# Kernel tuning notes

Measured on AMD Instinct MI355X. Metric: run time of the kernel, lower is better.

## Reference

```python
import jax, jax.numpy as jnp
import numpy as np

G = 4          # n_groups
KG = 1         # kernel_groups[stage]
KS = 8         # kernel_sizes[stage]
EIN = 64       # eff_in_dim = in_dim // n_groups
EOUT = 64      # eff_out_dim
PIN = 32       # in_points
POUT = 128     # out_points
QD = 256       # query_dim
EPS = 1e-5


def _ln(x, axes):
    m = jnp.mean(x, axis=axes, keepdims=True)
    v = jnp.var(x, axis=axes, keepdims=True)
    return (x - m) * jax.lax.rsqrt(v + EPS)


def setup_inputs() -> dict:
    key = jax.random.key(0)
    ks = jax.random.split(key, 14)
    B, N = 8, 300
    s = 0.02
    common_out = G * (EIN * EOUT + PIN * POUT)  # 32768
    priv_out = 2 * G * KG * KS * KS             # 512
    flat = EOUT * POUT * G                      # 32768
    return {
        "stage": 0,
        "x": jax.random.normal(ks[0], (B, N, G, PIN, EIN), jnp.float32),
        "query": jax.random.normal(ks[1], (B, N, QD), jnp.float32),
        "cpg_w": jax.random.normal(ks[2], (common_out, QD), jnp.float32) * s,
        "cpg_b": jax.random.normal(ks[3], (common_out,), jnp.float32) * s,
        "ppg_w": jax.random.normal(ks[4], (priv_out, QD), jnp.float32) * s,
        "ppg_b": jax.random.normal(ks[5], (priv_out,), jnp.float32) * s,
        "ml": jax.random.normal(ks[6], (G * KG, EIN, KS), jnp.float32) * 0.1,
        "mr": jax.random.normal(ks[7], (G * KG, KS, EOUT), jnp.float32) * 0.1,
        "sl": jax.random.normal(ks[8], (G * KG, POUT, KS), jnp.float32) * 0.1,
        "sr": jax.random.normal(ks[9], (G * KG, KS, PIN), jnp.float32) * 0.1,
        "base_w": jax.random.normal(ks[10], (QD, flat), jnp.float32) * s,
        "lora_A": jax.random.normal(ks[11], (64, flat), jnp.float32) * s,
        "lora_B": jax.random.normal(ks[12], (QD, 64), jnp.float32) * s,
        "out_bias": jnp.zeros((QD,), jnp.float32),
        "gamma": jnp.ones((QD,), jnp.float32),
        "beta": jnp.zeros((QD,), jnp.float32),
    }


def reference(stage, x, query, cpg_w, cpg_b, ppg_w, ppg_b, ml, mr, sl, sr,
              base_w, lora_A, lora_B, out_bias, gamma, beta):
    B, N, g, P, C = x.shape
    BN = B * N
    q = query.reshape(BN, QD)

    # common (query-generated) mixing params
    common = (q @ cpg_w.T + cpg_b).reshape(BN, G, EIN * EOUT + PIN * POUT)
    Mc = common[..., : EIN * EOUT].reshape(BN, G, EIN, EOUT)
    Sc = common[..., EIN * EOUT :].reshape(BN, G, POUT, PIN)

    # private factorized params: ml @ mz @ mr, sl @ sz @ sr
    priv = (q @ ppg_w.T + ppg_b).reshape(BN, 2, G * KG, KS, KS)
    mz, sz = priv[:, 0], priv[:, 1]
    Mp = jnp.einsum("gik,bgkl,glj->bgij", ml, mz, mr)  # (BN, G*KG, EIN, EOUT)
    Sp = jnp.einsum("gik,bgkl,glj->bgij", sl, sz, sr)  # (BN, G*KG, POUT, PIN)

    M = Mc + Mp.reshape(BN, G, KG, EIN, EOUT).sum(axis=2)
    S = Sc + Sp.reshape(BN, G, KG, POUT, PIN).sum(axis=2)

    out = x.reshape(BN, G, P, C)
    # adaptive channel mixing + LN over last two dims + ReLU
    out = jnp.einsum("bgpc,bgcd->bgpd", out, M)
    out = jax.nn.relu(_ln(out, (-2, -1)))
    # adaptive spatial mixing + LN + ReLU
    out = jnp.einsum("bgop,bgpd->bgod", S, out)  # (BN, G, POUT, EOUT)
    out = jax.nn.relu(_ln(out, (-2, -1)))

    # low-rank-adjusted linear projection to query dim
    out = out.reshape(B, N, G * POUT * EOUT)
    W = base_w + lora_B @ lora_A  # (QD, flat)
    out = out @ W.T + out_bias

    # residual + affine LayerNorm
    y = query + out
    return _ln(y, (-1,)) * gamma + beta
```

## Files before the change

kernel.cpp:

```cpp
#include <hip/hip_runtime.h>
#include <hip/hip_bf16.h>

#define BN_TOK 2400
#define QDIM   256
#define NG     4
#define FLAT   32768
#define GSZ    8192
#define KSP    16
#define LN_EPS 1e-5f
#define PPAD   42

typedef __attribute__((ext_vector_type(8))) short bf16x8;
typedef __attribute__((ext_vector_type(4))) float f32x4;
typedef __hip_bfloat16 bf16;

__device__ __forceinline__ float bf2f(ushort u) {
  union { unsigned int i; float f; } c;
  c.i = ((unsigned int)u) << 16;
  return c.f;
}
__device__ __forceinline__ ushort f2u(float f) {
  bf16 h = __float2bfloat16(f);
  union { bf16 h; ushort u; } c; c.h = h; return c.u;
}

__device__ __forceinline__ int xcdswz(int orig, int nwg) {
  int xcd = orig & 7, base = orig >> 3;
  int q = nwg >> 3, r = nwg & 7;
  int start = (xcd < r) ? xcd * (q + 1) : r * (q + 1) + (xcd - r) * q;
  return start + base;
}

__global__ __launch_bounds__(256) void cast_k(const float* __restrict__ in,
                                              bf16* __restrict__ out, int n4) {
  int i = blockIdx.x * 256 + threadIdx.x;
  if (i < n4) {
    float4 v = ((const float4*)in)[i];
    bf16 tmp[4] = {__float2bfloat16(v.x), __float2bfloat16(v.y),
                   __float2bfloat16(v.z), __float2bfloat16(v.w)};
    ((ushort4*)out)[i] = *(const ushort4*)tmp;
  }
}

__global__ __launch_bounds__(256) void build_weff_k(
    const float* __restrict__ cpg_w, const float* __restrict__ cpg_b,
    const float* __restrict__ ppg_w, const float* __restrict__ ppg_b,
    const float* __restrict__ ml, const float* __restrict__ mr,
    const float* __restrict__ sl, const float* __restrict__ sr,
    bf16* __restrict__ Weff, float* __restrict__ bias_eff) {
  int tid = threadIdx.x;
  int rb = blockIdx.x;
  int g = blockIdx.y;
  int part = blockIdx.z;
  int pbase = part * 256 + g * 64;

  float pw[64];
#pragma unroll
  for (int kl = 0; kl < 64; ++kl)
    pw[kl] = ppg_w[(size_t)(pbase + kl) * QDIM + tid];

  if (part == 0) {
    int d = rb;
    float t[8];
#pragma unroll
    for (int k = 0; k < 8; ++k) {
      float s = 0.f;
#pragma unroll
      for (int l = 0; l < 8; ++l) s += mr[g * 512 + l * 64 + d] * pw[k * 8 + l];
      t[k] = s;
    }
    for (int r = 0; r < 64; ++r) {
      int outrow = g * GSZ + d * 64 + r;
      int srcrow = g * GSZ + r * 64 + d;
      float acc = cpg_w[(size_t)srcrow * QDIM + tid];
#pragma unroll
      for (int k = 0; k < 8; ++k) acc += ml[g * 512 + r * 8 + k] * t[k];
      Weff[(size_t)outrow * QDIM + tid] = __float2bfloat16(acc);
    }
    if (tid < 64) {
      int r = tid;
      float b = cpg_b[g * GSZ + r * 64 + d];
#pragma unroll
      for (int k = 0; k < 8; ++k) {
        float s = 0.f;
#pragma unroll
        for (int l = 0; l < 8; ++l)
          s += mr[g * 512 + l * 64 + d] * ppg_b[pbase + k * 8 + l];
        b += ml[g * 512 + r * 8 + k] * s;
      }
      bias_eff[g * GSZ + d * 64 + r] = b;
    }
  } else {
    int o0 = rb * 2;
    float t0v[8], t1v[8];
#pragma unroll
    for (int l = 0; l < 8; ++l) {
      float s0 = 0.f, s1 = 0.f;
#pragma unroll
      for (int k = 0; k < 8; ++k) {
        s0 += sl[g * 1024 + o0 * 8 + k] * pw[k * 8 + l];
        s1 += sl[g * 1024 + (o0 + 1) * 8 + k] * pw[k * 8 + l];
      }
      t0v[l] = s0; t1v[l] = s1;
    }
    for (int r = 0; r < 32; ++r) {
      int rr = rb * 64 + r;
      int p = rr & 31;
      int row = g * GSZ + 4096 + rr;
      float acc = cpg_w[(size_t)row * QDIM + tid];
#pragma unroll
      for (int l = 0; l < 8; ++l) acc += sr[g * 256 + l * 32 + p] * t0v[l];
      Weff[(size_t)row * QDIM + tid] = __float2bfloat16(acc);
    }
    for (int r = 32; r < 64; ++r) {
      int rr = rb * 64 + r;
      int p = rr & 31;
      int row = g * GSZ + 4096 + rr;
      float acc = cpg_w[(size_t)row * QDIM + tid];
#pragma unroll
      for (int l = 0; l < 8; ++l) acc += sr[g * 256 + l * 32 + p] * t1v[l];
      Weff[(size_t)row * QDIM + tid] = __float2bfloat16(acc);
    }
    if (tid < 64) {
      int rr = rb * 64 + tid;
      int o = rr >> 5, p = rr & 31;
      int row = g * GSZ + 4096 + rr;
      float b = cpg_b[row];
#pragma unroll
      for (int l = 0; l < 8; ++l) {
        float s = 0.f;
#pragma unroll
        for (int k = 0; k < 8; ++k)
          s += sl[g * 1024 + o * 8 + k] * ppg_b[pbase + k * 8 + l];
        b += sr[g * 256 + l * 32 + p] * s;
      }
      bias_eff[row] = b;
    }
  }
}

__global__ __launch_bounds__(256) void build_wb_k(
    const float* __restrict__ base_w, const float* __restrict__ lora_A,
    const float* __restrict__ lora_B, bf16* __restrict__ Wb) {
  int jb = blockIdx.x * 256;
  int i0 = blockIdx.y * 16;
  int tid = threadIdx.x;
  __shared__ float lB[16][64];
  for (int e = tid; e < 16 * 64; e += 256)
    lB[e >> 6][e & 63] = lora_B[(size_t)(i0 + (e >> 6)) * 64 + (e & 63)];
  __syncthreads();
  int j = jb + tid;
  float acc[16] = {};
  for (int r = 0; r < 64; ++r) {
    float la = lora_A[(size_t)r * FLAT + j];
#pragma unroll
    for (int i = 0; i < 16; ++i) acc[i] += lB[i][r] * la;
  }
#pragma unroll
  for (int i = 0; i < 16; ++i)
    Wb[(size_t)(i0 + i) * FLAT + j] =
        __float2bfloat16(base_w[(size_t)(i0 + i) * FLAT + j] + acc[i]);
}

template <bool OBF>
__global__ __launch_bounds__(256) void gemm_nt(
    const bf16* __restrict__ A, const bf16* __restrict__ B,
    const float* __restrict__ bias, void* __restrict__ Cout,
    int M, int lda, int ldb, int Kslice, int ldc) {
  __shared__ __align__(16) ushort smem[16384];
  ushort* As = smem;
  ushort* Bs = smem + 8192;
  int tid = threadIdx.x;
  int w = tid >> 6, lane = tid & 63;
  int nwg = gridDim.x * gridDim.y;
  int swz = xcdswz(blockIdx.x + gridDim.x * blockIdx.y, nwg);
  int m0 = (swz % gridDim.x) * 128, n0 = (swz / gridDim.x) * 128;
  int kbase = blockIdx.z * Kslice;
  int wm = (w & 1) * 64, wn = (w >> 1) * 64;
  f32x4 acc[4][4] = {};
  for (int kb = 0; kb < Kslice; kb += 64) {
#pragma unroll
    for (int i = 0; i < 4; ++i) {
      int c = (i * 4 + w) * 64 + lane;
      int row = c >> 3, slot = c & 7;
      int ss = slot ^ (row & 7);
      int grow = m0 + row; if (grow >= M) grow = M - 1;
      const bf16* srcA = A + (size_t)grow * lda + kbase + kb + ss * 8;
      __builtin_amdgcn_global_load_lds(
          (const __attribute__((address_space(1))) void*)srcA,
          (__attribute__((address_space(3))) void*)(As + (size_t)c * 8), 16, 0, 0);
      const bf16* srcB = B + (size_t)(n0 + row) * ldb + kbase + kb + ss * 8;
      __builtin_amdgcn_global_load_lds(
          (const __attribute__((address_space(1))) void*)srcB,
          (__attribute__((address_space(3))) void*)(Bs + (size_t)c * 8), 16, 0, 0);
    }
    __syncthreads();
#pragma unroll
    for (int ks = 0; ks < 2; ++ks) {
      int sl = ks * 4 + (lane >> 4);
      bf16x8 af[4], bfr[4];
#pragma unroll
      for (int i = 0; i < 4; ++i) {
        int r = wm + i * 16 + (lane & 15);
        af[i] = *(const bf16x8*)&As[r * 64 + (sl ^ (r & 7)) * 8];
        int cc = wn + i * 16 + (lane & 15);
        bfr[i] = *(const bf16x8*)&Bs[cc * 64 + (sl ^ (cc & 7)) * 8];
      }
#pragma unroll
      for (int i = 0; i < 4; ++i)
#pragma unroll
        for (int j = 0; j < 4; ++j)
          acc[i][j] = __builtin_amdgcn_mfma_f32_16x16x32_bf16(bfr[j], af[i], acc[i][j], 0, 0, 0);
    }
    __syncthreads();
  }

  if constexpr (OBF) {
#pragma unroll
    for (int i = 0; i < 4; ++i) {
      int row = wm + i * 16 + (lane & 15);
#pragma unroll
      for (int j = 0; j < 4; ++j) {
        int nl = wn + j * 16 + (lane >> 4) * 4;
        float4 b4 = bias ? *(const float4*)&bias[n0 + nl] : make_float4(0.f, 0.f, 0.f, 0.f);
        ushort4 uv = {f2u(acc[i][j][0] + b4.x), f2u(acc[i][j][1] + b4.y),
                      f2u(acc[i][j][2] + b4.z), f2u(acc[i][j][3] + b4.w)};
        *(ushort4*)&smem[row * 128 + (nl ^ ((row & 7) << 3))] = uv;
      }
    }
    __syncthreads();
    bf16* co = (bf16*)Cout;
#pragma unroll
    for (int it = 0; it < 8; ++it) {
      int row = it * 16 + (tid >> 4);
      int sub = (tid & 15) * 8;
      int gm = m0 + row;
      if (gm < M) {
        *(bf16x8*)(co + ((size_t)blockIdx.z * M + gm) * ldc + n0 + sub) =
            *(const bf16x8*)&smem[row * 128 + (sub ^ ((row & 7) << 3))];
      }
    }
  } else {
#pragma unroll
    for (int i = 0; i < 4; ++i) {
      int m = m0 + wm + i * 16 + (lane & 15);
      if (m >= M) continue;
      size_t ro = (size_t)blockIdx.z * M + m;
#pragma unroll
      for (int j = 0; j < 4; ++j) {
        int nb = n0 + wn + j * 16 + (lane >> 4) * 4;
        float4 b4 = bias ? *(const float4*)&bias[nb] : make_float4(0.f, 0.f, 0.f, 0.f);
        *(float4*)((float*)Cout + ro * ldc + nb) =
            make_float4(acc[i][j][0] + b4.x, acc[i][j][1] + b4.y,
                        acc[i][j][2] + b4.z, acc[i][j][3] + b4.w);
      }
    }
  }
}

__device__ __forceinline__ void block_red2(float& s, float& sq, float* redS,
                                           float* redQ, int tid) {
#pragma unroll
  for (int off = 32; off > 0; off >>= 1) {
    s += __shfl_down(s, off);
    sq += __shfl_down(sq, off);
  }
  int w = tid >> 6;
  if ((tid & 63) == 0) { redS[w] = s; redQ[w] = sq; }
  __syncthreads();
  s = redS[0] + redS[1] + redS[2] + redS[3];
  sq = redQ[0] + redQ[1] + redQ[2] + redQ[3];
}

__global__ __launch_bounds__(256) void chain_k(
    const float* __restrict__ x, bf16* __restrict__ common) {
  int tid = threadIdx.x;
  int tl = blockIdx.x;
  int g = blockIdx.y;
  int lane = tid & 63, w = tid >> 6;

  __shared__ __align__(16) ushort sm[14720];
  __shared__ float redS[4], redQ[4];
  ushort* Mt = sm;
  ushort* Ss = sm + 4608;
  ushort* xbs = sm + 9728;
  ushort* o1Tb = sm + 12032;

  bf16* cm = common + (size_t)tl * FLAT + g * GSZ;
  const ushort* cmu = (const ushort*)cm;
  const float* xg = x + ((size_t)tl * NG + g) * 2048;

#pragma unroll
  for (int it = 0; it < 2; ++it) {
    int idx = it * 256 + tid;
    int e = idx * 8;
    {
      bf16x8 v = *(const bf16x8*)&cmu[e];
      *(bf16x8*)&Mt[(e >> 6) * 72 + (e & 63)] = v;
    }
    {
      bf16x8 v = *(const bf16x8*)&cmu[4096 + e];
      *(bf16x8*)&Ss[(e >> 5) * 40 + (e & 31)] = v;
    }
    {
      int fi = it * 256 + tid;
      float4 v = ((const float4*)xg)[fi];
      int fl = fi * 4;
      ushort4 u = {f2u(v.x), f2u(v.y), f2u(v.z), f2u(v.w)};
      *(ushort4*)&xbs[(fl >> 6) * 72 + (fl & 63)] = u;
    }
  }
  __syncthreads();

  int dlane = w * 16 + (lane & 15);
  f32x4 a1[2] = {};
#pragma unroll
  for (int ks = 0; ks < 2; ++ks) {
    bf16x8 af = *(const bf16x8*)&Mt[dlane * 72 + ks * 32 + (lane >> 4) * 8];
#pragma unroll
    for (int pt = 0; pt < 2; ++pt) {
      int p = pt * 16 + (lane & 15);
      bf16x8 bx = *(const bf16x8*)&xbs[p * 72 + ks * 32 + (lane >> 4) * 8];
      a1[pt] = __builtin_amdgcn_mfma_f32_16x16x32_bf16(af, bx, a1[pt], 0, 0, 0);
    }
  }
  {
    float s = 0.f, sq = 0.f;
#pragma unroll
    for (int pt = 0; pt < 2; ++pt)
#pragma unroll
      for (int r = 0; r < 4; ++r) { float v = a1[pt][r]; s += v; sq += v * v; }
    block_red2(s, sq, redS, redQ, tid);
    float mean = s * (1.f / 2048.f);
    float var = sq * (1.f / 2048.f) - mean * mean;
    float rs = rsqrtf(var + LN_EPS);
#pragma unroll
    for (int pt = 0; pt < 2; ++pt)
#pragma unroll
      for (int r = 0; r < 4; ++r) {
        float v = (a1[pt][r] - mean) * rs;
        if (v < 0.f) v = 0.f;
        int d = w * 16 + (lane >> 4) * 4 + r;
        int p = pt * 16 + (lane & 15);
        o1Tb[d * PPAD + p] = f2u(v);
      }
  }
  __syncthreads();

  f32x4 a2[2][4] = {};
  {
    bf16x8 bfd[4];
#pragma unroll
    for (int dj = 0; dj < 4; ++dj)
      bfd[dj] = *(const bf16x8*)&o1Tb[(dj * 16 + (lane & 15)) * PPAD + (lane >> 4) * 8];
#pragma unroll
    for (int oi = 0; oi < 2; ++oi) {
      int o = (2 * w + oi) * 16 + (lane & 15);
      bf16x8 sf = *(const bf16x8*)&Ss[o * 40 + (lane >> 4) * 8];
#pragma unroll
      for (int dj = 0; dj < 4; ++dj)
        a2[oi][dj] = __builtin_amdgcn_mfma_f32_16x16x32_bf16(bfd[dj], sf, a2[oi][dj], 0, 0, 0);
    }
  }
  {
    float s = 0.f, sq = 0.f;
#pragma unroll
    for (int oi = 0; oi < 2; ++oi)
#pragma unroll
      for (int dj = 0; dj < 4; ++dj)
#pragma unroll
        for (int r = 0; r < 4; ++r) { float v = a2[oi][dj][r]; s += v; sq += v * v; }
    block_red2(s, sq, redS, redQ, tid);
    float mean = s * (1.f / 8192.f);
    float var = sq * (1.f / 8192.f) - mean * mean;
    float rs = rsqrtf(var + LN_EPS);
#pragma unroll
    for (int oi = 0; oi < 2; ++oi) {
      int o = (2 * w + oi) * 16 + (lane & 15);
#pragma unroll
      for (int dj = 0; dj < 4; ++dj) {
        int d0 = dj * 16 + (lane >> 4) * 4;
        ushort4 uv;
#pragma unroll
        for (int r = 0; r < 4; ++r) {
          float v = (a2[oi][dj][r] - mean) * rs;
          if (v < 0.f) v = 0.f;
          ((ushort*)&uv)[r] = f2u(v);
        }
        *(ushort4*)&sm[o * 72 + d0] = uv;
      }
    }
  }
  __syncthreads();
  {
    ushort* cw = (ushort*)cm;
#pragma unroll
    for (int it = 0; it < 4; ++it) {
      int e = (it * 256 + tid) * 8;
      *(bf16x8*)&cw[e] = *(const bf16x8*)&sm[(e >> 6) * 72 + (e & 63)];
    }
  }
}

__global__ __launch_bounds__(256) void finish_k(
    const float* __restrict__ partial, const float* __restrict__ query,
    const float* __restrict__ out_bias, const float* __restrict__ gamma,
    const float* __restrict__ beta, float* __restrict__ out, int t0, int M) {
  int tid = threadIdx.x;
  int tl = blockIdx.x;
  int t = t0 + tl;
  __shared__ float redS[4], redQ[4];
  float s = 0.f;
  for (int ks = 0; ks < KSP; ++ks)
    s += partial[((size_t)ks * M + tl) * QDIM + tid];
  float v = s + out_bias[tid] + query[(size_t)t * QDIM + tid];
  float sum = v, sqv = v * v;
  block_red2(sum, sqv, redS, redQ, tid);
  float mean = sum * (1.f / 256.f);
  float var = sqv * (1.f / 256.f) - mean * mean;
  out[(size_t)t * QDIM + tid] =
      (v - mean) * rsqrtf(var + LN_EPS) * gamma[tid] + beta[tid];
}

extern "C" void kernel_launch(void* const* d_in, const int* in_sizes, int n_in,
                              void* d_out, int out_size, void* d_ws, size_t ws_size,
                              hipStream_t stream) {
  const float* x       = (const float*)d_in[1];
  const float* query   = (const float*)d_in[2];
  const float* cpg_w   = (const float*)d_in[3];
  const float* cpg_b   = (const float*)d_in[4];
  const float* ppg_w   = (const float*)d_in[5];
  const float* ppg_b   = (const float*)d_in[6];
  const float* ml      = (const float*)d_in[7];
  const float* mr      = (const float*)d_in[8];
  const float* sl      = (const float*)d_in[9];
  const float* sr      = (const float*)d_in[10];
  const float* base_w  = (const float*)d_in[11];
  const float* lora_A  = (const float*)d_in[12];
  const float* lora_B  = (const float*)d_in[13];
  const float* out_bias= (const float*)d_in[14];
  const float* gamma   = (const float*)d_in[15];
  const float* beta    = (const float*)d_in[16];
  float* out = (float*)d_out;

  float* wsf = (float*)d_ws;
  bf16*  Wb      = (bf16*)(wsf + 0);
  bf16*  Weff    = (bf16*)(wsf + 4194304);
  float* bias_eff= wsf + 8388608;
  bf16*  qb      = (bf16*)(wsf + 8421376);
  size_t fixedF  = 8728576;
  int CT = (ws_size >= (fixedF + (size_t)BN_TOK * 20480) * sizeof(float)) ? BN_TOK : 600;
  int NCH = BN_TOK / CT;
  bf16*  commonb = (bf16*)(wsf + fixedF);
  float* partialb= wsf + fixedF + (size_t)CT * 16384;

  build_weff_k<<<dim3(64, NG, 2), 256, 0, stream>>>(
      cpg_w, cpg_b, ppg_w, ppg_b, ml, mr, sl, sr, Weff, bias_eff);
  cast_k<<<dim3(BN_TOK * QDIM / 4 / 256), 256, 0, stream>>>(query, qb, BN_TOK * QDIM / 4);
  build_wb_k<<<dim3(FLAT / 256, QDIM / 16), 256, 0, stream>>>(base_w, lora_A, lora_B, Wb);

  for (int ch = 0; ch < NCH; ++ch) {
    int t0 = ch * CT;
    gemm_nt<true><<<dim3((CT + 127) / 128, FLAT / 128, 1), 256, 0, stream>>>(
        qb + (size_t)t0 * QDIM, Weff, bias_eff, commonb, CT, QDIM, QDIM, QDIM, FLAT);
    chain_k<<<dim3(CT, NG), 256, 0, stream>>>(x + (size_t)t0 * GSZ, commonb);
    gemm_nt<false><<<dim3((CT + 127) / 128, QDIM / 128, KSP), 256, 0, stream>>>(
        commonb, Wb, nullptr, partialb, CT, FLAT, FLAT, FLAT / KSP, QDIM);
    finish_k<<<dim3(CT), 256, 0, stream>>>(partialb, query, out_bias, gamma, beta, out, t0, CT);
  }
}
```

Before: 284.6 us.

## Enlarge GEMM tile to 256x128 and double split-K factor

```diff
diff --git a/kernel.cpp b/kernel.cpp
--- a/kernel.cpp
+++ b/kernel.cpp
@@ -6,7 +6,7 @@
 #define NG     4
 #define FLAT   32768
 #define GSZ    8192
-#define KSP    16
+#define KSP    32
 #define LN_EPS 1e-5f
 #define PPAD   42
 
@@ -167,20 +167,20 @@
     const bf16* __restrict__ A, const bf16* __restrict__ B,
     const float* __restrict__ bias, void* __restrict__ Cout,
     int M, int lda, int ldb, int Kslice, int ldc) {
-  __shared__ __align__(16) ushort smem[16384];
+  __shared__ __align__(16) ushort smem[24576];
   ushort* As = smem;
-  ushort* Bs = smem + 8192;
+  ushort* Bs = smem + 16384;
   int tid = threadIdx.x;
   int w = tid >> 6, lane = tid & 63;
   int nwg = gridDim.x * gridDim.y;
   int swz = xcdswz(blockIdx.x + gridDim.x * blockIdx.y, nwg);
-  int m0 = (swz % gridDim.x) * 128, n0 = (swz / gridDim.x) * 128;
+  int m0 = (swz % gridDim.x) * 256, n0 = (swz / gridDim.x) * 128;
   int kbase = blockIdx.z * Kslice;
-  int wm = (w & 1) * 64, wn = (w >> 1) * 64;
-  f32x4 acc[4][4] = {};
+  f32x4 acc[4][8] = {};
+
   for (int kb = 0; kb < Kslice; kb += 64) {
 #pragma unroll
-    for (int i = 0; i < 4; ++i) {
+    for (int i = 0; i < 8; ++i) {
       int c = (i * 4 + w) * 64 + lane;
       int row = c >> 3, slot = c & 7;
       int ss = slot ^ (row & 7);
@@ -189,6 +189,12 @@
       __builtin_amdgcn_global_load_lds(
           (const __attribute__((address_space(1))) void*)srcA,
           (__attribute__((address_space(3))) void*)(As + (size_t)c * 8), 16, 0, 0);
+    }
+#pragma unroll
+    for (int i = 0; i < 4; ++i) {
+      int c = (i * 4 + w) * 64 + lane;
+      int row = c >> 3, slot = c & 7;
+      int ss = slot ^ (row & 7);
       const bf16* srcB = B + (size_t)(n0 + row) * ldb + kbase + kb + ss * 8;
       __builtin_amdgcn_global_load_lds(
           (const __attribute__((address_space(1))) void*)srcB,
@@ -198,18 +204,21 @@
 #pragma unroll
     for (int ks = 0; ks < 2; ++ks) {
       int sl = ks * 4 + (lane >> 4);
-      bf16x8 af[4], bfr[4];
+      bf16x8 af[4], bfr[8];
 #pragma unroll
       for (int i = 0; i < 4; ++i) {
-        int r = wm + i * 16 + (lane & 15);
+        int r = w * 64 + i * 16 + (lane & 15);
         af[i] = *(const bf16x8*)&As[r * 64 + (sl ^ (r & 7)) * 8];
-        int cc = wn + i * 16 + (lane & 15);
-        bfr[i] = *(const bf16x8*)&Bs[cc * 64 + (sl ^ (cc & 7)) * 8];
+      }
+#pragma unroll
+      for (int j = 0; j < 8; ++j) {
+        int cc = j * 16 + (lane & 15);
+        bfr[j] = *(const bf16x8*)&Bs[cc * 64 + (sl ^ (cc & 7)) * 8];
       }
 #pragma unroll
       for (int i = 0; i < 4; ++i)
 #pragma unroll
-        for (int j = 0; j < 4; ++j)
+        for (int j = 0; j < 8; ++j)
           acc[i][j] = __builtin_amdgcn_mfma_f32_16x16x32_bf16(bfr[j], af[i], acc[i][j], 0, 0, 0);
     }
     __syncthreads();
@@ -217,38 +226,45 @@
 
   if constexpr (OBF) {
 #pragma unroll
+    for (int h = 0; h < 2; ++h) {
+      if ((w >> 1) == h) {
+        int wl = w & 1;
+#pragma unroll
+        for (int i = 0; i < 4; ++i) {
+          int row = wl * 64 + i * 16 + (lane & 15);
+#pragma unroll
+          for (int j = 0; j < 8; ++j) {
+            int nl = j * 16 + (lane >> 4) * 4;
+            float4 b4 = bias ? *(const float4*)&bias[n0 + nl] : make_float4(0.f, 0.f, 0.f, 0.f);
+            ushort4 uv = {f2u(acc[i][j][0] + b4.x), f2u(acc[i][j][1] + b4.y),
+                          f2u(acc[i][j][2] + b4.z), f2u(acc[i][j][3] + b4.w)};
+            *(ushort4*)&smem[row * 128 + (nl ^ ((row & 7) << 3))] = uv;
+          }
+        }
+      }
+      __syncthreads();
+      bf16* co = (bf16*)Cout;
+#pragma unroll
+      for (int it = 0; it < 8; ++it) {
+        int row = it * 16 + (tid >> 4);
+        int sub = (tid & 15) * 8;
+        int gm = m0 + h * 128 + row;
+        if (gm < M) {
+          *(bf16x8*)(co + ((size_t)blockIdx.z * M + gm) * ldc + n0 + sub) =
+              *(const bf16x8*)&smem[row * 128 + (sub ^ ((row & 7) << 3))];
+        }
+      }
+      __syncthreads();
+    }
+  } else {
+#pragma unroll
     for (int i = 0; i < 4; ++i) {
-      int row = wm + i * 16 + (lane & 15);
-#pragma unroll
-      for (int j = 0; j < 4; ++j) {
-        int nl = wn + j * 16 + (lane >> 4) * 4;
-        float4 b4 = bias ? *(const float4*)&bias[n0 + nl] : make_float4(0.f, 0.f, 0.f, 0.f);
-        ushort4 uv = {f2u(acc[i][j][0] + b4.x), f2u(acc[i][j][1] + b4.y),
-                      f2u(acc[i][j][2] + b4.z), f2u(acc[i][j][3] + b4.w)};
-        *(ushort4*)&smem[row * 128 + (nl ^ ((row & 7) << 3))] = uv;
-      }
-    }
-    __syncthreads();
-    bf16* co = (bf16*)Cout;
-#pragma unroll
-    for (int it = 0; it < 8; ++it) {
-      int row = it * 16 + (tid >> 4);
-      int sub = (tid & 15) * 8;
-      int gm = m0 + row;
-      if (gm < M) {
-        *(bf16x8*)(co + ((size_t)blockIdx.z * M + gm) * ldc + n0 + sub) =
-            *(const bf16x8*)&smem[row * 128 + (sub ^ ((row & 7) << 3))];
-      }
-    }
-  } else {
-#pragma unroll
-    for (int i = 0; i < 4; ++i) {
-      int m = m0 + wm + i * 16 + (lane & 15);
+      int m = m0 + w * 64 + i * 16 + (lane & 15);
       if (m >= M) continue;
       size_t ro = (size_t)blockIdx.z * M + m;
 #pragma unroll
-      for (int j = 0; j < 4; ++j) {
-        int nb = n0 + wn + j * 16 + (lane >> 4) * 4;
+      for (int j = 0; j < 8; ++j) {
+        int nb = n0 + j * 16 + (lane >> 4) * 4;
         float4 b4 = bias ? *(const float4*)&bias[nb] : make_float4(0.f, 0.f, 0.f, 0.f);
         *(float4*)((float*)Cout + ro * ldc + nb) =
             make_float4(acc[i][j][0] + b4.x, acc[i][j][1] + b4.y,
@@ -449,7 +465,7 @@
   float* bias_eff= wsf + 8388608;
   bf16*  qb      = (bf16*)(wsf + 8421376);
   size_t fixedF  = 8728576;
-  int CT = (ws_size >= (fixedF + (size_t)BN_TOK * 20480) * sizeof(float)) ? BN_TOK : 600;
+  int CT = (ws_size >= (fixedF + (size_t)BN_TOK * 24576) * sizeof(float)) ? BN_TOK : 600;
   int NCH = BN_TOK / CT;
   bf16*  commonb = (bf16*)(wsf + fixedF);
   float* partialb= wsf + fixedF + (size_t)CT * 16384;
@@ -461,10 +477,10 @@
 
   for (int ch = 0; ch < NCH; ++ch) {
     int t0 = ch * CT;
-    gemm_nt<true><<<dim3((CT + 127) / 128, FLAT / 128, 1), 256, 0, stream>>>(
+    gemm_nt<true><<<dim3((CT + 255) / 256, FLAT / 128, 1), 256, 0, stream>>>(
         qb + (size_t)t0 * QDIM, Weff, bias_eff, commonb, CT, QDIM, QDIM, QDIM, FLAT);
     chain_k<<<dim3(CT, NG), 256, 0, stream>>>(x + (size_t)t0 * GSZ, commonb);
-    gemm_nt<false><<<dim3((CT + 127) / 128, QDIM / 128, KSP), 256, 0, stream>>>(
+    gemm_nt<false><<<dim3((CT + 255) / 256, QDIM / 128, KSP), 256, 0, stream>>>(
         commonb, Wb, nullptr, partialb, CT, FLAT, FLAT, FLAT / KSP, QDIM);
     finish_k<<<dim3(CT), 256, 0, stream>>>(partialb, query, out_bias, gamma, beta, out, t0, CT);
   }
```

Measured after the change: 430.1 us. +51.2%, slower.
